# Performance work log

Measured on AMD Instinct MI355X. Metric: run time of the kernel, lower is better.

## Reference

```python
import jax, jax.numpy as jnp
import numpy as np

B, DIM, KEY_DIM, NH, AR, RES, KS = 32, 512, 16, 8, 4, 64, 5
D = AR * KEY_DIM          # 64, per-head value dim
C4 = DIM // 4             # 128, q/k channel dim
CHUNK = DIM // NH         # 64, per-head input chunk
SCALE = KEY_DIM ** -0.5


def setup_inputs() -> dict:
    key = jax.random.key(0)
    ks = jax.random.split(key, 8)
    def rn(k, shape, fan):
        return jax.random.normal(k, shape, jnp.float32) * (fan ** -0.5)
    x = jax.random.normal(ks[0], (B, DIM, RES, RES), jnp.float32)
    qk_w = rn(ks[1], (DIM // 2, DIM), DIM)            # fused 1x1 conv+BN weight
    qk_b = jnp.zeros((DIM // 2,), jnp.float32)
    dws_w = rn(ks[2], (C4, 1, KS, KS), KS * KS)        # depthwise conv weight
    dws_b = jnp.zeros((C4,), jnp.float32)
    vs_w = rn(ks[3], (NH, D, CHUNK), CHUNK)            # per-head 1x1 conv weights
    vs_b = jnp.zeros((NH, D), jnp.float32)
    proj_w = rn(ks[4], (DIM, D * NH), D * NH)
    proj_b = jnp.zeros((DIM,), jnp.float32)
    bias_h = jax.random.normal(ks[5], (1, RES), jnp.float32) * 0.02
    bias_w = jax.random.normal(ks[6], (1, RES), jnp.float32) * 0.02
    # offset id for (p1, p2) is exactly |p1 - p2| given enumeration order
    idx = jnp.abs(jnp.arange(RES)[:, None] - jnp.arange(RES)[None, :]).astype(jnp.int32)
    return dict(x=x, qk_w=qk_w, qk_b=qk_b, dws_w=dws_w, dws_b=dws_b,
                vs_w=vs_w, vs_b=vs_b, proj_w=proj_w, proj_b=proj_b,
                bias_h=bias_h, bias_w=bias_w, idx_h=idx, idx_w=idx)


def reference(x, qk_w, qk_b, dws_w, dws_b, vs_w, vs_b, proj_w, proj_b,
              bias_h, bias_w, idx_h, idx_w):
    ab_h = bias_h[0][idx_h]                               # [N, N]
    ab_w = bias_w[0][idx_w]                               # [N, N]
    # qk: fused 1x1 conv + BN -> [B, C/2, H, W]
    feat = jnp.einsum('oc,bchw->bohw', qk_w, x) + qk_b[None, :, None, None]
    q, k = feat[:, :C4], feat[:, C4:]
    # depthwise 5x5 conv on q
    q = jax.lax.conv_general_dilated(
        q, dws_w, (1, 1), 'SAME',
        dimension_numbers=('NCHW', 'OIHW', 'NCHW'),
        feature_group_count=C4) + dws_b[None, :, None, None]
    qr_w = jnp.transpose(q, (0, 2, 3, 1))                 # [B, H, W, C4]
    kr_w = jnp.transpose(k, (0, 2, 3, 1))                 # [B, H, W, C4]
    attn_w = jax.nn.softmax(
        jnp.einsum('bhqc,bhkc->bhqk', qr_w, kr_w) * SCALE + ab_w, axis=-1)
    qr_h = jnp.transpose(qr_w, (0, 2, 1, 3))              # [B, W, H, C4]
    kr_h = jnp.transpose(kr_w, (0, 2, 1, 3))
    attn_h = jax.nn.softmax(
        jnp.einsum('bwqc,bwkc->bwqk', qr_h, kr_h) * SCALE + ab_h, axis=-1)
    # cascaded per-head value chain
    feats_out = []
    feat_i = x[:, :CHUNK]
    for i in range(NH):
        if i > 0:
            feat_i = feat_i + x[:, i * CHUNK:(i + 1) * CHUNK]
        v = jnp.einsum('dc,bchw->bdhw', vs_w[i], feat_i) + vs_b[i][None, :, None, None]
        v = jnp.transpose(v, (0, 2, 3, 1))                # [B, H, W, d]
        v = jnp.einsum('bhqk,bhkd->bhqd', attn_w, v)      # attend along W
        v = jnp.transpose(v, (0, 2, 1, 3))                # [B, W, H, d]
        f = jnp.einsum('bwqk,bwkd->bwqd', attn_h, v)      # attend along H
        feats_out.append(jnp.transpose(f, (0, 3, 2, 1)))  # [B, d, H, W]
    out = jnp.concatenate(feats_out, axis=1)              # [B, d*NH, H, W]
    out = jax.nn.relu(out)
    out = jnp.einsum('oc,bchw->bohw', proj_w, out) + proj_b[None, :, None, None]
    return out
```

## Files before the change

### kernel.cpp

```cpp
#include <hip/hip_runtime.h>

#define PIX 4096
#define SCALE 0.25f

typedef _Float16 f16x8 __attribute__((ext_vector_type(8)));
typedef float f32x4 __attribute__((ext_vector_type(4)));

__device__ inline void gload_lds16(const _Float16* g, _Float16* l) {
  __builtin_amdgcn_global_load_lds((const __attribute__((address_space(1))) void*)g,
                                   (__attribute__((address_space(3))) void*)l, 16, 0, 0);
}

__global__ __launch_bounds__(256) void k_cvt(const float* __restrict__ in,
                                             _Float16* __restrict__ out, int n) {
  int i = blockIdx.x * 256 + threadIdx.x;
  if (i < n) out[i] = (_Float16)in[i];
}

__global__ __launch_bounds__(256) void k_build_wbig(const float* __restrict__ vs_w,
                                                    _Float16* __restrict__ Wbig) {
  int row = blockIdx.x;
  int i = row >> 6, d = row & 63;
  for (int col = threadIdx.x; col < 512; col += 256) {
    int j = col >> 6, c = col & 63;
    Wbig[row * 512 + col] = (j <= i) ? (_Float16)vs_w[i * 4096 + d * 64 + c] : (_Float16)0;
  }
}

__global__ __launch_bounds__(256) void k_xt(const float* __restrict__ x,
                                            _Float16* __restrict__ xh) {
  __shared__ float tile[64][65];
  int b = blockIdx.z, k0 = blockIdx.y * 64, p0 = blockIdx.x * 64;
  const float* xp = x + ((size_t)b * 512 + k0) * PIX + p0;
  _Float16* out = xh + (size_t)b * PIX * 512;
  int t = threadIdx.x;
  int r = t >> 4, c4 = (t & 15) << 2;
#pragma unroll
  for (int it = 0; it < 4; ++it) {
    float4 v = *(const float4*)&xp[(size_t)(r + it * 16) * PIX + c4];
    tile[r + it * 16][c4 + 0] = v.x; tile[r + it * 16][c4 + 1] = v.y;
    tile[r + it * 16][c4 + 2] = v.z; tile[r + it * 16][c4 + 3] = v.w;
  }
  __syncthreads();
  int pr = t >> 5, kk = (t & 31) << 1;
#pragma unroll
  for (int it = 0; it < 8; ++it) {
    int p = pr + it * 8;
    union { _Float16 h[2]; unsigned int u; } pk;
    pk.h[0] = (_Float16)tile[kk][p]; pk.h[1] = (_Float16)tile[kk + 1][p];
    *(unsigned int*)&out[(size_t)(p0 + p) * 512 + k0 + kk] = pk.u;
  }
}

template<int MODE>
__global__ __launch_bounds__(512, 2) void k_mg8(const _Float16* __restrict__ A,
                                                const _Float16* __restrict__ B,
                                                const float* __restrict__ bias,
                                                const _Float16* __restrict__ attn,
                                                float* C, _Float16* H, int nwg_m) {
  __shared__ __align__(16) _Float16 lds[65536];
  int nwg = gridDim.x;
  int id = blockIdx.x;
  int qq = nwg >> 3;
  id = (id & 7) * qq + (id >> 3);
  int mb = id % nwg_m;
  int rest = id / nwg_m;
  int pb = rest & 15;
  int b  = rest >> 4;
  int m0 = mb * 256, p0 = pb * 256;
  int t = threadIdx.x, wid = t >> 6, lane = t & 63;
  int wm = wid >> 2, wn = wid & 3;
  int lr = lane & 15, q4 = lane >> 4;
  const _Float16* Ab = A + (size_t)m0 * 512;
  const _Float16* Bp = B + (size_t)b * 2097152 + (size_t)p0 * 512;

  int nt = (MODE == 1) ? ((m0 + 256) >> 6) : 8;
  int nsub = nt * 2;

  auto STAGE = [&](int g) {
    int slot = g & 3;
    _Float16* dA = lds + slot * 16384;
    _Float16* dB = dA + 8192;
    size_t ks = (size_t)g * 32;
#pragma unroll
    for (int is = 0; is < 2; ++is) {
      int L = is * 512 + wid * 64 + lane;
      int row = L >> 2, sl = L & 3;
      int c = sl ^ ((row >> 1) & 3);
      gload_lds16(Ab + (size_t)row * 512 + ks + c * 8, dA + (size_t)(is * 512 + wid * 64) * 8);
      gload_lds16(Bp + (size_t)row * 512 + ks + c * 8, dB + (size_t)(is * 512 + wid * 64) * 8);
    }
  };

  f32x4 acc[8][4] = {};
  STAGE(0); STAGE(1); STAGE(2);
  for (int n = 0; n < nsub; ++n) {
    if (n + 3 < nsub) STAGE(n + 3);
    int r = nsub - 1 - n; if (r > 3) r = 3;
    if (r == 3)      asm volatile("s_waitcnt vmcnt(12)" ::: "memory");
    else if (r == 2) asm volatile("s_waitcnt vmcnt(8)" ::: "memory");
    else if (r == 1) asm volatile("s_waitcnt vmcnt(4)" ::: "memory");
    else             asm volatile("s_waitcnt vmcnt(0)" ::: "memory");
    __builtin_amdgcn_s_barrier();
    const _Float16* A_s = lds + (n & 3) * 16384;
    const _Float16* B_s = A_s + 8192;
    f16x8 af[8], bf[4];
#pragma unroll
    for (int mi = 0; mi < 8; ++mi) {
      int row = wm * 128 + mi * 16 + lr;
      af[mi] = *(const f16x8*)&A_s[row * 32 + ((q4 ^ ((row >> 1) & 3)) << 3)];
    }
#pragma unroll
    for (int ni = 0; ni < 4; ++ni) {
      int row = wn * 64 + ni * 16 + lr;
      bf[ni] = *(const f16x8*)&B_s[row * 32 + ((q4 ^ ((row >> 1) & 3)) << 3)];
    }
    __builtin_amdgcn_s_setprio(1);
#pragma unroll
    for (int mi = 0; mi < 8; ++mi)
#pragma unroll
      for (int ni = 0; ni < 4; ++ni)
        acc[mi][ni] = __builtin_amdgcn_mfma_f32_16x16x32_f16(af[mi], bf[ni], acc[mi][ni], 0, 0, 0);
    __builtin_amdgcn_s_setprio(0);
    __builtin_amdgcn_s_barrier();
  }

  if (MODE == 0) {
#pragma unroll
    for (int mi = 0; mi < 8; ++mi)
#pragma unroll
      for (int rr = 0; rr < 4; ++rr) {
        int m = m0 + wm * 128 + mi * 16 + q4 * 4 + rr;
        float bi = bias[m];
        float* crow = C + ((size_t)b * 512 + m) * PIX + p0 + wn * 64;
#pragma unroll
        for (int ni = 0; ni < 4; ++ni)
          crow[ni * 16 + lr] = acc[mi][ni][rr] + bi;
      }
  }

  if (MODE == 1) {
    _Float16* Cs = lds + wid * 8192;
#pragma unroll
    for (int mi = 0; mi < 8; ++mi)
#pragma unroll
      for (int ni = 0; ni < 4; ++ni)
#pragma unroll
        for (int rr = 0; rr < 4; ++rr) {
          int row = mi * 16 + q4 * 4 + rr;
          int col = ni * 16 + lr;
          Cs[row * 64 + ((((col >> 3) ^ (row & 7)) << 3) | (col & 7))] =
              (_Float16)(acc[mi][ni][rr] + bias[m0 + wm * 128 + row]);
        }
    int s = pb * 4 + wn;
    const _Float16* Ab2 = attn + ((size_t)b * 64 + s) * 4096;
    f16x8 bfr[4][2];
#pragma unroll
    for (int ni = 0; ni < 4; ++ni)
#pragma unroll
      for (int kk = 0; kk < 2; ++kk)
        bfr[ni][kk] = *(const f16x8*)&Ab2[(ni * 16 + lr) * 64 + q4 * 8 + kk * 32];
    f32x4 acc2[8][4] = {};
#pragma unroll
    for (int mi2 = 0; mi2 < 8; ++mi2)
#pragma unroll
      for (int kk = 0; kk < 2; ++kk) {
        int row = mi2 * 16 + lr;
        f16x8 afr = *(const f16x8*)&Cs[row * 64 + (((q4 + kk * 4) ^ (row & 7)) << 3)];
#pragma unroll
        for (int ni2 = 0; ni2 < 4; ++ni2)
          acc2[mi2][ni2] = __builtin_amdgcn_mfma_f32_16x16x32_f16(afr, bfr[ni2][kk], acc2[mi2][ni2], 0, 0, 0);
      }
#pragma unroll
    for (int mi2 = 0; mi2 < 8; ++mi2)
#pragma unroll
      for (int rr = 0; rr < 4; ++rr) {
        int m = m0 + wm * 128 + mi2 * 16 + q4 * 4 + rr;
        _Float16* crow = H + ((size_t)b * 512 + m) * PIX + p0 + wn * 64;
#pragma unroll
        for (int ni2 = 0; ni2 < 4; ++ni2)
          crow[ni2 * 16 + lr] = (_Float16)acc2[mi2][ni2][rr];
      }
  }

  if (MODE == 2) {
    if (wm == 0) {
#pragma unroll
      for (int mi = 0; mi < 8; ++mi)
#pragma unroll
        for (int rr = 0; rr < 4; ++rr) {
          int m = mi * 16 + q4 * 4 + rr;
          float bi = bias[m];
          float* crow = C + ((size_t)b * 128 + m) * PIX + p0 + wn * 64;
#pragma unroll
          for (int ni = 0; ni < 4; ++ni)
            crow[ni * 16 + lr] = acc[mi][ni][rr] + bi;
        }
    } else {
      _Float16* Ls = lds + (size_t)(wid - 4) * 16384;
#pragma unroll
      for (int mi = 0; mi < 8; ++mi)
#pragma unroll
        for (int ni = 0; ni < 4; ++ni)
#pragma unroll
          for (int rr = 0; rr < 4; ++rr) {
            int ch = mi * 16 + q4 * 4 + rr;
            Ls[(ni * 16 + lr) * 136 + ch] = (_Float16)(acc[mi][ni][rr] + bias[128 + ch]);
          }
      _Float16* khb = H + ((size_t)b * PIX + p0 + wn * 64) * 128;
#pragma unroll
      for (int it = 0; it < 16; ++it) {
        int chk = it * 64 + lane;
        int prow = chk >> 4, cc = (chk & 15) << 3;
        *(f16x8*)&khb[(size_t)prow * 128 + cc] = *(const f16x8*)&Ls[prow * 136 + cc];
      }
    }
  }
}

__global__ __launch_bounds__(256) void k_dwconv(const float* __restrict__ feat,
                                                const float* __restrict__ w,
                                                const float* __restrict__ bias,
                                                float* __restrict__ qconv) {
  __shared__ float tile[68][68];
  int c = blockIdx.x, b = blockIdx.y;
  const float* in = feat + ((size_t)b * 128 + c) * PIX;
  float wreg[25];
#pragma unroll
  for (int i = 0; i < 25; ++i) wreg[i] = w[c * 25 + i];
  float bi = bias[c];
  int t = threadIdx.x;
  for (int idx = t; idx < 68 * 68; idx += 256) {
    int y = idx / 68, xx = idx - y * 68;
    int h = y - 2, ww = xx - 2;
    float v = 0.f;
    if (h >= 0 && h < 64 && ww >= 0 && ww < 64) v = in[h * 64 + ww];
    tile[y][xx] = v;
  }
  __syncthreads();
  float* out = qconv + ((size_t)b * 128 + c) * PIX;
  int tx = (t & 15) << 2, ty = (t >> 4) << 2;
#pragma unroll
  for (int i = 0; i < 4; ++i) {
    float4 o;
    float* po = (float*)&o;
#pragma unroll
    for (int j = 0; j < 4; ++j) {
      float s = bi;
#pragma unroll
      for (int dy = 0; dy < 5; ++dy)
#pragma unroll
        for (int dx = 0; dx < 5; ++dx)
          s += wreg[dy * 5 + dx] * tile[ty + i + dy][tx + j + dx];
      po[j] = s;
    }
    *(float4*)&out[(ty + i) * 64 + tx] = o;
  }
}

__global__ __launch_bounds__(256) void k_qkt(const float* __restrict__ in, long ibs, int ic0,
                                             _Float16* __restrict__ out) {
  __shared__ __align__(16) _Float16 Ts[64 * 136];
  int p0 = blockIdx.x * 64, b = blockIdx.y;
  const float* ip = in + (size_t)b * ibs + (size_t)ic0 * PIX;
  int t = threadIdx.x;
#pragma unroll
  for (int it = 0; it < 8; ++it) {
    int i4 = it * 256 + t;
    int c = i4 >> 4, pp = (i4 & 15) << 2;
    float4 v = *(const float4*)&ip[(size_t)c * PIX + p0 + pp];
    Ts[(pp + 0) * 136 + c] = (_Float16)v.x;
    Ts[(pp + 1) * 136 + c] = (_Float16)v.y;
    Ts[(pp + 2) * 136 + c] = (_Float16)v.z;
    Ts[(pp + 3) * 136 + c] = (_Float16)v.w;
  }
  __syncthreads();
  _Float16* op = out + (size_t)b * (PIX * 128) + (size_t)p0 * 128;
#pragma unroll
  for (int it = 0; it < 4; ++it) {
    int ch = it * 256 + t;
    int p = ch >> 4, cc = (ch & 15) << 3;
    *(f16x8*)&op[p * 128 + cc] = *(const f16x8*)&Ts[p * 136 + cc];
  }
}

__global__ __launch_bounds__(256) void k_mattn(const _Float16* __restrict__ qh,
                                               const _Float16* __restrict__ kh,
                                               const float* __restrict__ bias_w,
                                               const float* __restrict__ bias_h,
                                               _Float16* __restrict__ attnW,
                                               _Float16* __restrict__ attnH) {
  __shared__ __align__(16) _Float16 Qs[64 * 136];
  __shared__ __align__(16) _Float16 Ks[64 * 136];
  __shared__ float bl[64];
  int j = blockIdx.x, b = blockIdx.y, which = blockIdx.z;
  const float* bias = which ? bias_h : bias_w;
  _Float16* attn = which ? attnH : attnW;
  int t = threadIdx.x;
  if (t < 64) bl[t] = bias[t];
  const _Float16* qb = qh + (size_t)b * (PIX * 128);
  const _Float16* kb = kh + (size_t)b * (PIX * 128);
#pragma unroll
  for (int it = 0; it < 4; ++it) {
    int idx = it * 256 + t;
    int r = idx >> 4, cc = (idx & 15) << 3;
    size_t p = which ? (size_t)(j + 64 * r) : (size_t)(j * 64 + r);
    *(f16x8*)&Qs[r * 136 + cc] = *(const f16x8*)&qb[p * 128 + cc];
    *(f16x8*)&Ks[r * 136 + cc] = *(const f16x8*)&kb[p * 128 + cc];
  }
  __syncthreads();
  int wave = t >> 6, lane = t & 63;
  int lr = lane & 15, q4 = lane >> 4;
  f16x8 af[4];
#pragma unroll
  for (int kk = 0; kk < 4; ++kk)
    af[kk] = *(const f16x8*)&Qs[(wave * 16 + lr) * 136 + q4 * 8 + kk * 32];
  f32x4 acc[4] = {};
#pragma unroll
  for (int ni = 0; ni < 4; ++ni)
#pragma unroll
    for (int kk = 0; kk < 4; ++kk) {
      f16x8 bf = *(const f16x8*)&Ks[(ni * 16 + lr) * 136 + q4 * 8 + kk * 32];
      acc[ni] = __builtin_amdgcn_mfma_f32_16x16x32_f16(af[kk], bf, acc[ni], 0, 0, 0);
    }
  float ev[4][4], sm[4];
#pragma unroll
  for (int r = 0; r < 4; ++r) {
    int qrow = wave * 16 + q4 * 4 + r;
    float m = -1e30f;
#pragma unroll
    for (int ni = 0; ni < 4; ++ni) {
      int k = ni * 16 + lr;
      ev[ni][r] = acc[ni][r] * SCALE + bl[abs(qrow - k)];
      m = fmaxf(m, ev[ni][r]);
    }
    m = fmaxf(m, __shfl_xor(m, 1)); m = fmaxf(m, __shfl_xor(m, 2));
    m = fmaxf(m, __shfl_xor(m, 4)); m = fmaxf(m, __shfl_xor(m, 8));
    float s = 0.f;
#pragma unroll
    for (int ni = 0; ni < 4; ++ni) { ev[ni][r] = __expf(ev[ni][r] - m); s += ev[ni][r]; }
    s += __shfl_xor(s, 1); s += __shfl_xor(s, 2);
    s += __shfl_xor(s, 4); s += __shfl_xor(s, 8);
    sm[r] = 1.f / s;
  }
  _Float16* ab = attn + (((size_t)b * 64 + j) * 64) * 64;
#pragma unroll
  for (int r = 0; r < 4; ++r) {
    int qrow = wave * 16 + q4 * 4 + r;
#pragma unroll
    for (int ni = 0; ni < 4; ++ni)
      ab[qrow * 64 + ni * 16 + lr] = (_Float16)(ev[ni][r] * sm[r]);
  }
}

__global__ __launch_bounds__(256) void k_hmix(const _Float16* __restrict__ tT,
                                              const _Float16* __restrict__ attnH,
                                              _Float16* __restrict__ ght) {
  __shared__ __align__(16) _Float16 Ts[128 * 64];
  __shared__ __align__(16) _Float16 Ls[64 * 136];
  int id = blockIdx.x;
  int ct = id & 3, w = (id >> 2) & 63, b = id >> 8;
  int t = threadIdx.x, wid = t >> 6, lane = t & 63;
  int lr = lane & 15, q4 = lane >> 4;
  const _Float16* Tb = tT + ((size_t)b * 512 + ct * 128) * PIX + w * 64;
#pragma unroll
  for (int it = 0; it < 4; ++it) {
    int idx = it * 256 + t;
    int row = idx >> 3, c = idx & 7;
    int sc = c ^ (row & 7);
    gload_lds16(Tb + (size_t)row * PIX + sc * 8, &Ts[(it * 256 + wid * 64) * 8]);
  }
  const _Float16* Ab = attnH + ((size_t)b * 64 + w) * 4096;
  f16x8 bfr[4][2];
#pragma unroll
  for (int ni = 0; ni < 4; ++ni)
#pragma unroll
    for (int kk = 0; kk < 2; ++kk)
      bfr[ni][kk] = *(const f16x8*)&Ab[(ni * 16 + lr) * 64 + q4 * 8 + kk * 32];
  __syncthreads();
  f32x4 acc[2][4] = {};
#pragma unroll
  for (int mi = 0; mi < 2; ++mi) {
    int rr = wid * 32 + mi * 16 + lr;
#pragma unroll
    for (int kk = 0; kk < 2; ++kk) {
      f16x8 af = *(const f16x8*)&Ts[rr * 64 + (((q4 + 4 * kk) ^ (rr & 7)) << 3)];
#pragma unroll
      for (int ni = 0; ni < 4; ++ni)
        acc[mi][ni] = __builtin_amdgcn_mfma_f32_16x16x32_f16(af, bfr[ni][kk], acc[mi][ni], 0, 0, 0);
    }
  }
#pragma unroll
  for (int mi = 0; mi < 2; ++mi)
#pragma unroll
    for (int ni = 0; ni < 4; ++ni)
#pragma unroll
      for (int rr = 0; rr < 4; ++rr) {
        float v = acc[mi][ni][rr];
        Ls[(ni * 16 + lr) * 136 + wid * 32 + mi * 16 + q4 * 4 + rr] =
            (_Float16)(v > 0.f ? v : 0.f);
      }
  __syncthreads();
  _Float16* gb = ght + (size_t)b * PIX * 512 + ct * 128;
#pragma unroll
  for (int it = 0; it < 4; ++it) {
    int idx = it * 256 + t;
    int hp = idx >> 4, cc = (idx & 15) << 3;
    *(f16x8*)&gb[((size_t)hp * 64 + w) * 512 + cc] = *(const f16x8*)&Ls[hp * 136 + cc];
  }
}

__global__ __launch_bounds__(256) void k_t16(const _Float16* __restrict__ in,
                                             _Float16* __restrict__ out) {
  __shared__ _Float16 tile[64][65];
  int img = blockIdx.x;
  const _Float16* ip = in + (size_t)img * PIX;
  _Float16* op = out + (size_t)img * PIX;
  int t = threadIdx.x;
  int col = t & 63, r0 = t >> 6;
  for (int it = 0; it < 16; ++it) {
    int r = r0 + it * 4;
    tile[r][col] = ip[r * 64 + col];
  }
  __syncthreads();
  for (int it = 0; it < 16; ++it) {
    int r = r0 + it * 4;
    op[r * 64 + col] = tile[col][r];
  }
}

extern "C" void kernel_launch(void* const* d_in, const int* in_sizes, int n_in,
                              void* d_out, int out_size, void* d_ws, size_t ws_size,
                              hipStream_t stream) {
  const float* x      = (const float*)d_in[0];
  const float* qk_w   = (const float*)d_in[1];
  const float* qk_b   = (const float*)d_in[2];
  const float* dws_w  = (const float*)d_in[3];
  const float* dws_b  = (const float*)d_in[4];
  const float* vs_w   = (const float*)d_in[5];
  const float* vs_b   = (const float*)d_in[6];
  const float* proj_w = (const float*)d_in[7];
  const float* proj_b = (const float*)d_in[8];
  const float* bias_h = (const float*)d_in[9];
  const float* bias_w = (const float*)d_in[10];

  float* ws = (float*)d_ws;
  float* dout = (float*)d_out;

  _Float16* xh    = (_Float16*)ws;
  _Float16* ght   = xh;
  float*    feat  = ws + 33554432;
  _Float16* tT    = (_Float16*)(ws + 33554432);
  _Float16* attnW = (_Float16*)(ws + 67108864);
  _Float16* attnH = (_Float16*)(ws + 71303168);
  _Float16* qkw_h  = (_Float16*)(ws + 75497472);
  _Float16* wbig_h = (_Float16*)(ws + 75563008);
  _Float16* pjw_h  = (_Float16*)(ws + 75694080);

  float*    qconv = dout;
  _Float16* qh    = (_Float16*)(dout + 16777216);
  _Float16* kh    = (_Float16*)(dout + 25165824);
  _Float16* Vh    = (_Float16*)(dout + 33554432);

  k_cvt<<<dim3(512), 256, 0, stream>>>(qk_w, qkw_h, 131072);
  k_cvt<<<dim3(1024), 256, 0, stream>>>(proj_w, pjw_h, 262144);
  k_build_wbig<<<512, 256, 0, stream>>>(vs_w, wbig_h);
  k_xt<<<dim3(64, 8, 32), 256, 0, stream>>>(x, xh);
  k_mg8<2><<<512, 512, 0, stream>>>(qkw_h, xh, qk_b, nullptr, feat, kh, 1);
  k_dwconv<<<dim3(128, 32), 256, 0, stream>>>(feat, dws_w, dws_b, qconv);
  k_qkt<<<dim3(64, 32), 256, 0, stream>>>(qconv, 128L * PIX, 0, qh);
  k_mattn<<<dim3(64, 32, 2), 256, 0, stream>>>(qh, kh, bias_w, bias_h, attnW, attnH);
  k_mg8<1><<<1024, 512, 0, stream>>>(wbig_h, xh, vs_b, attnW, nullptr, Vh, 2);
  k_t16<<<32 * 512, 256, 0, stream>>>(Vh, tT);
  k_hmix<<<8192, 256, 0, stream>>>(tT, attnH, ght);
  k_mg8<0><<<1024, 512, 0, stream>>>(pjw_h, ght, proj_b, nullptr, dout, nullptr, 2);
}
```

Baseline: 601.5 us.

## Fuse V transpose into value GEMM epilogue, halve M tile, fp16 q intermediates

The value GEMM (MODE 1) now uses 128-row M tiles and twice as many workgroups. Its epilogue stages results in LDS and writes them already transposed, which removes the separate k_t16 transpose kernel and its extra global round trip. The q-feature path (qk GEMM output, depthwise conv output, q transpose input) moves from fp32 to fp16 storage, halving that memory traffic. Smaller tiles cut per-workgroup A reuse, and the fp16 intermediates could reduce accuracy slightly.

New measurement: 632.8 us. 5.2% more time.

```diff
diff --git a/kernel.cpp b/kernel.cpp
--- a/kernel.cpp
+++ b/kernel.cpp
@@ -4,6 +4,7 @@
 #define SCALE 0.25f
 
 typedef _Float16 f16x8 __attribute__((ext_vector_type(8)));
+typedef _Float16 f16x4 __attribute__((ext_vector_type(4)));
 typedef float f32x4 __attribute__((ext_vector_type(4)));
 
 __device__ inline void gload_lds16(const _Float16* g, _Float16* l) {
@@ -57,7 +58,12 @@
                                                 const _Float16* __restrict__ B,
                                                 const float* __restrict__ bias,
                                                 const _Float16* __restrict__ attn,
-                                                float* C, _Float16* H, int nwg_m) {
+                                                float* C, _Float16* H, _Float16* H2,
+                                                int nwg_m) {
+  constexpr int MROWS = (MODE == 1) ? 128 : 256;
+  constexpr int AH = MROWS * 32;
+  constexpr int SLOT = AH + 8192;
+  constexpr int MI = MROWS / 32;
   __shared__ __align__(16) _Float16 lds[65536];
   int nwg = gridDim.x;
   int id = blockIdx.x;
@@ -67,47 +73,67 @@
   int rest = id / nwg_m;
   int pb = rest & 15;
   int b  = rest >> 4;
-  int m0 = mb * 256, p0 = pb * 256;
+  int m0 = mb * MROWS, p0 = pb * 256;
   int t = threadIdx.x, wid = t >> 6, lane = t & 63;
   int wm = wid >> 2, wn = wid & 3;
   int lr = lane & 15, q4 = lane >> 4;
   const _Float16* Ab = A + (size_t)m0 * 512;
   const _Float16* Bp = B + (size_t)b * 2097152 + (size_t)p0 * 512;
 
-  int nt = (MODE == 1) ? ((m0 + 256) >> 6) : 8;
+  int nt = (MODE == 1) ? ((m0 + 128) >> 6) : 8;
   int nsub = nt * 2;
 
   auto STAGE = [&](int g) {
     int slot = g & 3;
-    _Float16* dA = lds + slot * 16384;
-    _Float16* dB = dA + 8192;
+    _Float16* dA = lds + slot * SLOT;
+    _Float16* dB = dA + AH;
     size_t ks = (size_t)g * 32;
+    if constexpr (MODE == 1) {
+      int L = wid * 64 + lane;
+      int row = L >> 2, sl = L & 3;
+      int c = sl ^ ((row >> 1) & 3);
+      gload_lds16(Ab + (size_t)row * 512 + ks + c * 8, dA + (size_t)(wid * 64) * 8);
+    } else {
+#pragma unroll
+      for (int is = 0; is < 2; ++is) {
+        int L = is * 512 + wid * 64 + lane;
+        int row = L >> 2, sl = L & 3;
+        int c = sl ^ ((row >> 1) & 3);
+        gload_lds16(Ab + (size_t)row * 512 + ks + c * 8, dA + (size_t)(is * 512 + wid * 64) * 8);
+      }
+    }
 #pragma unroll
     for (int is = 0; is < 2; ++is) {
       int L = is * 512 + wid * 64 + lane;
       int row = L >> 2, sl = L & 3;
       int c = sl ^ ((row >> 1) & 3);
-      gload_lds16(Ab + (size_t)row * 512 + ks + c * 8, dA + (size_t)(is * 512 + wid * 64) * 8);
       gload_lds16(Bp + (size_t)row * 512 + ks + c * 8, dB + (size_t)(is * 512 + wid * 64) * 8);
     }
   };
 
-  f32x4 acc[8][4] = {};
+  f32x4 acc[MI][4] = {};
   STAGE(0); STAGE(1); STAGE(2);
   for (int n = 0; n < nsub; ++n) {
     if (n + 3 < nsub) STAGE(n + 3);
     int r = nsub - 1 - n; if (r > 3) r = 3;
-    if (r == 3)      asm volatile("s_waitcnt vmcnt(12)" ::: "memory");
-    else if (r == 2) asm volatile("s_waitcnt vmcnt(8)" ::: "memory");
-    else if (r == 1) asm volatile("s_waitcnt vmcnt(4)" ::: "memory");
-    else             asm volatile("s_waitcnt vmcnt(0)" ::: "memory");
+    if constexpr (MODE == 1) {
+      if (r == 3)      asm volatile("s_waitcnt vmcnt(9)" ::: "memory");
+      else if (r == 2) asm volatile("s_waitcnt vmcnt(6)" ::: "memory");
+      else if (r == 1) asm volatile("s_waitcnt vmcnt(3)" ::: "memory");
+      else             asm volatile("s_waitcnt vmcnt(0)" ::: "memory");
+    } else {
+      if (r == 3)      asm volatile("s_waitcnt vmcnt(12)" ::: "memory");
+      else if (r == 2) asm volatile("s_waitcnt vmcnt(8)" ::: "memory");
+      else if (r == 1) asm volatile("s_waitcnt vmcnt(4)" ::: "memory");
+      else             asm volatile("s_waitcnt vmcnt(0)" ::: "memory");
+    }
     __builtin_amdgcn_s_barrier();
-    const _Float16* A_s = lds + (n & 3) * 16384;
-    const _Float16* B_s = A_s + 8192;
-    f16x8 af[8], bf[4];
-#pragma unroll
-    for (int mi = 0; mi < 8; ++mi) {
-      int row = wm * 128 + mi * 16 + lr;
+    const _Float16* A_s = lds + (n & 3) * SLOT;
+    const _Float16* B_s = A_s + AH;
+    f16x8 af[MI], bf[4];
+#pragma unroll
+    for (int mi = 0; mi < MI; ++mi) {
+      int row = wm * (MROWS / 2) + mi * 16 + lr;
       af[mi] = *(const f16x8*)&A_s[row * 32 + ((q4 ^ ((row >> 1) & 3)) << 3)];
     }
 #pragma unroll
@@ -117,7 +143,7 @@
     }
     __builtin_amdgcn_s_setprio(1);
 #pragma unroll
-    for (int mi = 0; mi < 8; ++mi)
+    for (int mi = 0; mi < MI; ++mi)
 #pragma unroll
       for (int ni = 0; ni < 4; ++ni)
         acc[mi][ni] = __builtin_amdgcn_mfma_f32_16x16x32_f16(af[mi], bf[ni], acc[mi][ni], 0, 0, 0);
@@ -127,7 +153,7 @@
 
   if (MODE == 0) {
 #pragma unroll
-    for (int mi = 0; mi < 8; ++mi)
+    for (int mi = 0; mi < MI; ++mi)
 #pragma unroll
       for (int rr = 0; rr < 4; ++rr) {
         int m = m0 + wm * 128 + mi * 16 + q4 * 4 + rr;
@@ -140,9 +166,9 @@
   }
 
   if (MODE == 1) {
-    _Float16* Cs = lds + wid * 8192;
-#pragma unroll
-    for (int mi = 0; mi < 8; ++mi)
+    _Float16* Cs = lds + wid * 4096;
+#pragma unroll
+    for (int mi = 0; mi < 4; ++mi)
 #pragma unroll
       for (int ni = 0; ni < 4; ++ni)
 #pragma unroll
@@ -150,7 +176,7 @@
           int row = mi * 16 + q4 * 4 + rr;
           int col = ni * 16 + lr;
           Cs[row * 64 + ((((col >> 3) ^ (row & 7)) << 3) | (col & 7))] =
-              (_Float16)(acc[mi][ni][rr] + bias[m0 + wm * 128 + row]);
+              (_Float16)(acc[mi][ni][rr] + bias[m0 + wm * 64 + row]);
         }
     int s = pb * 4 + wn;
     const _Float16* Ab2 = attn + ((size_t)b * 64 + s) * 4096;
@@ -160,9 +186,9 @@
 #pragma unroll
       for (int kk = 0; kk < 2; ++kk)
         bfr[ni][kk] = *(const f16x8*)&Ab2[(ni * 16 + lr) * 64 + q4 * 8 + kk * 32];
-    f32x4 acc2[8][4] = {};
-#pragma unroll
-    for (int mi2 = 0; mi2 < 8; ++mi2)
+    f32x4 acc2[4][4] = {};
+#pragma unroll
+    for (int mi2 = 0; mi2 < 4; ++mi2)
 #pragma unroll
       for (int kk = 0; kk < 2; ++kk) {
         int row = mi2 * 16 + lr;
@@ -171,35 +197,44 @@
         for (int ni2 = 0; ni2 < 4; ++ni2)
           acc2[mi2][ni2] = __builtin_amdgcn_mfma_f32_16x16x32_f16(afr, bfr[ni2][kk], acc2[mi2][ni2], 0, 0, 0);
       }
-#pragma unroll
-    for (int mi2 = 0; mi2 < 8; ++mi2)
-#pragma unroll
-      for (int rr = 0; rr < 4; ++rr) {
-        int m = m0 + wm * 128 + mi2 * 16 + q4 * 4 + rr;
-        _Float16* crow = H + ((size_t)b * 512 + m) * PIX + p0 + wn * 64;
-#pragma unroll
-        for (int ni2 = 0; ni2 < 4; ++ni2)
-          crow[ni2 * 16 + lr] = (_Float16)acc2[mi2][ni2][rr];
-      }
+    _Float16* T = lds + 32768;
+#pragma unroll
+    for (int mi2 = 0; mi2 < 4; ++mi2)
+#pragma unroll
+      for (int ni2 = 0; ni2 < 4; ++ni2)
+#pragma unroll
+        for (int rr = 0; rr < 4; ++rr) {
+          int chl = wm * 64 + mi2 * 16 + q4 * 4 + rr;
+          int wp = ni2 * 16 + lr;
+          T[(chl * 64 + wp) * 4 + wn] = (_Float16)acc2[mi2][ni2][rr];
+        }
+    __syncthreads();
+    _Float16* tb = H + ((size_t)b * 512 + m0) * PIX + pb * 4;
+#pragma unroll
+    for (int it = 0; it < 16; ++it) {
+      int idx = it * 512 + t;
+      int ch = idx >> 6, wp = idx & 63;
+      *(f16x4*)&tb[(size_t)ch * PIX + wp * 64] = *(const f16x4*)&T[(ch * 64 + wp) * 4];
+    }
   }
 
   if (MODE == 2) {
     if (wm == 0) {
 #pragma unroll
-      for (int mi = 0; mi < 8; ++mi)
+      for (int mi = 0; mi < MI; ++mi)
 #pragma unroll
         for (int rr = 0; rr < 4; ++rr) {
           int m = mi * 16 + q4 * 4 + rr;
           float bi = bias[m];
-          float* crow = C + ((size_t)b * 128 + m) * PIX + p0 + wn * 64;
+          _Float16* crow = H2 + ((size_t)b * 128 + m) * PIX + p0 + wn * 64;
 #pragma unroll
           for (int ni = 0; ni < 4; ++ni)
-            crow[ni * 16 + lr] = acc[mi][ni][rr] + bi;
+            crow[ni * 16 + lr] = (_Float16)(acc[mi][ni][rr] + bi);
         }
     } else {
       _Float16* Ls = lds + (size_t)(wid - 4) * 16384;
 #pragma unroll
-      for (int mi = 0; mi < 8; ++mi)
+      for (int mi = 0; mi < MI; ++mi)
 #pragma unroll
         for (int ni = 0; ni < 4; ++ni)
 #pragma unroll
@@ -218,13 +253,13 @@
   }
 }
 
-__global__ __launch_bounds__(256) void k_dwconv(const float* __restrict__ feat,
+__global__ __launch_bounds__(256) void k_dwconv(const _Float16* __restrict__ feat,
                                                 const float* __restrict__ w,
                                                 const float* __restrict__ bias,
-                                                float* __restrict__ qconv) {
+                                                _Float16* __restrict__ qc) {
   __shared__ float tile[68][68];
   int c = blockIdx.x, b = blockIdx.y;
-  const float* in = feat + ((size_t)b * 128 + c) * PIX;
+  const _Float16* in = feat + ((size_t)b * 128 + c) * PIX;
   float wreg[25];
 #pragma unroll
   for (int i = 0; i < 25; ++i) wreg[i] = w[c * 25 + i];
@@ -234,16 +269,15 @@
     int y = idx / 68, xx = idx - y * 68;
     int h = y - 2, ww = xx - 2;
     float v = 0.f;
-    if (h >= 0 && h < 64 && ww >= 0 && ww < 64) v = in[h * 64 + ww];
+    if (h >= 0 && h < 64 && ww >= 0 && ww < 64) v = (float)in[h * 64 + ww];
     tile[y][xx] = v;
   }
   __syncthreads();
-  float* out = qconv + ((size_t)b * 128 + c) * PIX;
+  _Float16* out = qc + ((size_t)b * 128 + c) * PIX;
   int tx = (t & 15) << 2, ty = (t >> 4) << 2;
 #pragma unroll
   for (int i = 0; i < 4; ++i) {
-    float4 o;
-    float* po = (float*)&o;
+    f16x4 o;
 #pragma unroll
     for (int j = 0; j < 4; ++j) {
       float s = bi;
@@ -252,27 +286,25 @@
 #pragma unroll
         for (int dx = 0; dx < 5; ++dx)
           s += wreg[dy * 5 + dx] * tile[ty + i + dy][tx + j + dx];
-      po[j] = s;
-    }
-    *(float4*)&out[(ty + i) * 64 + tx] = o;
-  }
-}
-
-__global__ __launch_bounds__(256) void k_qkt(const float* __restrict__ in, long ibs, int ic0,
-                                             _Float16* __restrict__ out) {
+      o[j] = (_Float16)s;
+    }
+    *(f16x4*)&out[(ty + i) * 64 + tx] = o;
+  }
+}
+
+__global__ __launch_bounds__(256) void k_qkt16(const _Float16* __restrict__ in,
+                                               _Float16* __restrict__ out) {
   __shared__ __align__(16) _Float16 Ts[64 * 136];
   int p0 = blockIdx.x * 64, b = blockIdx.y;
-  const float* ip = in + (size_t)b * ibs + (size_t)ic0 * PIX;
+  const _Float16* ip = in + (size_t)b * 128 * PIX;
   int t = threadIdx.x;
 #pragma unroll
-  for (int it = 0; it < 8; ++it) {
+  for (int it = 0; it < 4; ++it) {
     int i4 = it * 256 + t;
-    int c = i4 >> 4, pp = (i4 & 15) << 2;
-    float4 v = *(const float4*)&ip[(size_t)c * PIX + p0 + pp];
-    Ts[(pp + 0) * 136 + c] = (_Float16)v.x;
-    Ts[(pp + 1) * 136 + c] = (_Float16)v.y;
-    Ts[(pp + 2) * 136 + c] = (_Float16)v.z;
-    Ts[(pp + 3) * 136 + c] = (_Float16)v.w;
+    int c = i4 >> 3, pc = (i4 & 7) << 3;
+    f16x8 v = *(const f16x8*)&ip[(size_t)c * PIX + p0 + pc];
+#pragma unroll
+    for (int j = 0; j < 8; ++j) Ts[(pc + j) * 136 + c] = v[j];
   }
   __syncthreads();
   _Float16* op = out + (size_t)b * (PIX * 128) + (size_t)p0 * 128;
@@ -410,25 +442,6 @@
   }
 }
 
-__global__ __launch_bounds__(256) void k_t16(const _Float16* __restrict__ in,
-                                             _Float16* __restrict__ out) {
-  __shared__ _Float16 tile[64][65];
-  int img = blockIdx.x;
-  const _Float16* ip = in + (size_t)img * PIX;
-  _Float16* op = out + (size_t)img * PIX;
-  int t = threadIdx.x;
-  int col = t & 63, r0 = t >> 6;
-  for (int it = 0; it < 16; ++it) {
-    int r = r0 + it * 4;
-    tile[r][col] = ip[r * 64 + col];
-  }
-  __syncthreads();
-  for (int it = 0; it < 16; ++it) {
-    int r = r0 + it * 4;
-    op[r * 64 + col] = tile[col][r];
-  }
-}
-
 extern "C" void kernel_launch(void* const* d_in, const int* in_sizes, int n_in,
                               void* d_out, int out_size, void* d_ws, size_t ws_size,
                               hipStream_t stream) {
@@ -449,7 +462,6 @@
 
   _Float16* xh    = (_Float16*)ws;
   _Float16* ght   = xh;
-  float*    feat  = ws + 33554432;
   _Float16* tT    = (_Float16*)(ws + 33554432);
   _Float16* attnW = (_Float16*)(ws + 67108864);
   _Float16* attnH = (_Float16*)(ws + 71303168);
@@ -457,21 +469,20 @@
   _Float16* wbig_h = (_Float16*)(ws + 75563008);
   _Float16* pjw_h  = (_Float16*)(ws + 75694080);
 
-  float*    qconv = dout;
-  _Float16* qh    = (_Float16*)(dout + 16777216);
-  _Float16* kh    = (_Float16*)(dout + 25165824);
-  _Float16* Vh    = (_Float16*)(dout + 33554432);
+  _Float16* feat_h = (_Float16*)dout;
+  _Float16* qc_h   = (_Float16*)(dout + 8388608);
+  _Float16* qh     = (_Float16*)(dout + 16777216);
+  _Float16* kh     = (_Float16*)(dout + 25165824);
 
   k_cvt<<<dim3(512), 256, 0, stream>>>(qk_w, qkw_h, 131072);
   k_cvt<<<dim3(1024), 256, 0, stream>>>(proj_w, pjw_h, 262144);
   k_build_wbig<<<512, 256, 0, stream>>>(vs_w, wbig_h);
   k_xt<<<dim3(64, 8, 32), 256, 0, stream>>>(x, xh);
-  k_mg8<2><<<512, 512, 0, stream>>>(qkw_h, xh, qk_b, nullptr, feat, kh, 1);
-  k_dwconv<<<dim3(128, 32), 256, 0, stream>>>(feat, dws_w, dws_b, qconv);
-  k_qkt<<<dim3(64, 32), 256, 0, stream>>>(qconv, 128L * PIX, 0, qh);
+  k_mg8<2><<<512, 512, 0, stream>>>(qkw_h, xh, qk_b, nullptr, nullptr, kh, feat_h, 1);
+  k_dwconv<<<dim3(128, 32), 256, 0, stream>>>(feat_h, dws_w, dws_b, qc_h);
+  k_qkt16<<<dim3(64, 32), 256, 0, stream>>>(qc_h, qh);
   k_mattn<<<dim3(64, 32, 2), 256, 0, stream>>>(qh, kh, bias_w, bias_h, attnW, attnH);
-  k_mg8<1><<<1024, 512, 0, stream>>>(wbig_h, xh, vs_b, attnW, nullptr, Vh, 2);
-  k_t16<<<32 * 512, 256, 0, stream>>>(Vh, tT);
+  k_mg8<1><<<2048, 512, 0, stream>>>(wbig_h, xh, vs_b, attnW, nullptr, tT, nullptr, 4);
   k_hmix<<<8192, 256, 0, stream>>>(tT, attnH, ght);
-  k_mg8<0><<<1024, 512, 0, stream>>>(pjw_h, ght, proj_b, nullptr, dout, nullptr, 2);
-}
+  k_mg8<0><<<1024, 512, 0, stream>>>(pjw_h, ght, proj_b, nullptr, dout, nullptr, nullptr, 2);
+}
```
